# Optimization experiments

Measured on AMD Instinct MI355X. Metric: run time of the kernel, lower is better.

Reference implementation:

```python
import jax, jax.numpy as jnp
import numpy as np

B, I, H = 8192, 1024, 1024

def setup_inputs() -> dict:
    key = jax.random.key(0)
    ks = jax.random.split(key, 5)
    # xavier-uniform-ish scale for weights
    sW = float(np.sqrt(6.0 / (I + H)))
    sU = float(np.sqrt(6.0 / (H + H)))
    return {
        "x": jax.random.normal(ks[0], (B, I), jnp.float32),
        "h": jax.random.normal(ks[1], (B, H), jnp.float32),
        "c": jax.random.normal(ks[2], (B, H), jnp.float32),
        # gate order along leading axis: 0=i, 1=f, 2=o, 3=c_hat
        "W": jax.random.uniform(ks[3], (4, H, I), jnp.float32, -sW, sW),
        "bW": jnp.zeros((4, H), jnp.float32),
        "U": jax.random.uniform(ks[4], (4, H, H), jnp.float32, -sU, sU),
        "bU": jnp.zeros((4, H), jnp.float32),
    }

def reference(x, h, c, W, bW, U, bU):
    # two batched GEMMs covering all 8 original Linear layers
    gx = jnp.einsum('bi,ghi->gbh', x, W) + bW[:, None, :]   # [4,B,H]
    gh = jnp.einsum('bk,ghk->gbh', h, U) + bU[:, None, :]   # [4,B,H]
    g = gx + gh
    i = jax.nn.sigmoid(g[0])
    f = jax.nn.sigmoid(g[1])
    o = jax.nn.sigmoid(g[2])
    c_hat = jnp.tanh(g[3])
    c_new = f * c + i * c_hat
    h_new = o * jnp.tanh(c_new)
    return (h_new, (h_new, c_new))
```

## Files before the change

kernel.cpp:

```cpp
#include <hip/hip_runtime.h>
#include <hip/hip_bf16.h>

typedef __hip_bfloat16 bf16;
typedef __attribute__((ext_vector_type(8))) short short8;
typedef __attribute__((ext_vector_type(4))) float floatx4;

#define B_DIM 8192
#define H_DIM 1024
#define KSUM 2048
#define BM 128
#define BN 128
#define BK 64
#define KITER 32
#define CEX_STRIDE 68

union BS { bf16 b; short s; };
__device__ __forceinline__ short cvt1(float f) {
  BS u; u.b = __float2bfloat16(f); return u.s;
}
__device__ __forceinline__ short8 cvt8(float4 lo, float4 hi) {
  short8 r;
  r[0] = cvt1(lo.x); r[1] = cvt1(lo.y); r[2] = cvt1(lo.z); r[3] = cvt1(lo.w);
  r[4] = cvt1(hi.x); r[5] = cvt1(hi.y); r[6] = cvt1(hi.z); r[7] = cvt1(hi.w);
  return r;
}

__device__ __forceinline__ void async_ld16(const bf16* g, bf16* lds) {
  __builtin_amdgcn_global_load_lds(
      (const __attribute__((address_space(1))) unsigned int*)g,
      (__attribute__((address_space(3))) unsigned int*)lds,
      16, 0, 0);
}

__global__ __launch_bounds__(256) void cvt_pack_A(
    const float* __restrict__ x, const float* __restrict__ h,
    bf16* __restrict__ Ac) {
  const int idx = blockIdx.x * 256 + threadIdx.x;
  const long row = idx >> 8;
  const int k0 = (idx & 255) << 3;
  const float* src = (k0 < 1024) ? (x + row * 1024 + k0)
                                 : (h + row * 1024 + (k0 - 1024));
  const float4 lo = *(const float4*)src;
  const float4 hi = *(const float4*)(src + 4);
  *(short8*)(Ac + row * KSUM + k0) = cvt8(lo, hi);
}

__global__ __launch_bounds__(256) void cvt_pack_B(
    const float* __restrict__ W, const float* __restrict__ U,
    bf16* __restrict__ Bc) {
  const int idx = blockIdx.x * 256 + threadIdx.x;
  const long r = idx >> 8;
  const int k0 = (idx & 255) << 3;
  const int g = (int)(r & 3);
  const long hh = r >> 2;
  const long base = (long)g * (H_DIM * H_DIM) + hh * H_DIM;
  const float* src = (k0 < 1024) ? (W + base + k0) : (U + base + (k0 - 1024));
  const float4 lo = *(const float4*)src;
  const float4 hi = *(const float4*)(src + 4);
  *(short8*)(Bc + r * KSUM + k0) = cvt8(lo, hi);
}

__device__ __forceinline__ float sigmoidf_(float v) {
  return 1.0f / (1.0f + __expf(-v));
}
__device__ __forceinline__ float tanhf_(float v) {
  return 1.0f - 2.0f / (__expf(2.0f * v) + 1.0f);
}
__device__ __forceinline__ float getc(const float4& v, int t) {
  return t == 0 ? v.x : t == 1 ? v.y : t == 2 ? v.z : v.w;
}

__global__ __launch_bounds__(256) void gemm_lstm(
    const bf16* __restrict__ Ac, const bf16* __restrict__ Bc,
    const float* __restrict__ cprev_g, const float* __restrict__ bW,
    const float* __restrict__ bU, float* __restrict__ out) {
  __shared__ __align__(16) char smem[32768];
  bf16* sA = (bf16*)smem;
  bf16* sB = (bf16*)(smem + 16384);
  float* cex = (float*)smem;

  const int tid  = threadIdx.x;
  const int lane = tid & 63;
  const int wv   = tid >> 6;

  const int blk  = blockIdx.x;
  const int xcd  = blk & 7;
  const int slot = blk >> 3;
  const int mt   = slot & 63;
  const int nt   = (xcd << 2) | (slot >> 6);
  const long m0 = (long)mt * BM;
  const long n0 = (long)nt * BN;

  const int lrow   = lane >> 3;
  const int lchunk = lane & 7;
  const int schunk = lchunk ^ lrow;
  const bf16* aSrc = Ac + (m0 + wv * 8 + lrow) * (long)KSUM + schunk * 8;
  const bf16* bSrc = Bc + (n0 + wv * 8 + lrow) * (long)KSUM + schunk * 8;
  bf16* sAw = sA + (wv * 8) * 64;
  bf16* sBw = sB + (wv * 8) * 64;

  const int wm = ((wv >> 1) & 1) << 6;
  const int wn = (wv & 1) << 6;
  const int col16 = lane & 15;
  const int quad  = lane >> 4;
  const int x7    = col16 & 7;

  floatx4 acc[4][4];
#pragma unroll
  for (int i = 0; i < 4; ++i)
#pragma unroll
    for (int j = 0; j < 4; ++j) acc[i][j] = (floatx4){0.f, 0.f, 0.f, 0.f};

  for (int kt = 0; kt < KITER; ++kt) {
    const long koff = (long)kt * BK;
    __syncthreads();
#pragma unroll
    for (int q = 0; q < 4; ++q) {
      async_ld16(aSrc + koff + (long)q * (32 * (long)KSUM), sAw + q * (32 * 64));
      async_ld16(bSrc + koff + (long)q * (32 * (long)KSUM), sBw + q * (32 * 64));
    }
    __syncthreads();

#pragma unroll
    for (int s = 0; s < 2; ++s) {
      const int cp = ((((s << 2) + quad) ^ x7) << 3);
      short8 af[4], bfr[4];
#pragma unroll
      for (int i = 0; i < 4; ++i) {
        af[i]  = *(const short8*)&sA[(wm + i * 16 + col16) * 64 + cp];
        bfr[i] = *(const short8*)&sB[(wn + i * 16 + col16) * 64 + cp];
      }
#pragma unroll
      for (int i = 0; i < 4; ++i)
#pragma unroll
        for (int j = 0; j < 4; ++j)
          acc[i][j] = __builtin_amdgcn_mfma_f32_16x16x32_bf16(af[i], bfr[j],
                                                              acc[i][j], 0, 0, 0);
    }
  }

  __syncthreads();

  const int rquad = (lane >> 4) << 2;
  const int row16 = lane & 15;
  const int tq    = lane >> 4;
  const long hglob = (n0 >> 2) + (wn >> 2) + tq * 4;

  float4 bsum[4];
#pragma unroll
  for (int g = 0; g < 4; ++g) {
    const float4 a = *(const float4*)(bW + g * H_DIM + hglob);
    const float4 b = *(const float4*)(bU + g * H_DIM + hglob);
    bsum[g] = (float4){a.x + b.x, a.y + b.y, a.z + b.z, a.w + b.w};
  }

  float* wx = cex + wv * (16 * CEX_STRIDE);
  const long BH = (long)B_DIM * H_DIM;

  for (int ig = 0; ig < 4; ++ig) {
#pragma unroll
    for (int j = 0; j < 4; ++j)
#pragma unroll
      for (int r = 0; r < 4; ++r)
        wx[(rquad + r) * CEX_STRIDE + j * 16 + col16] = acc[ig][j][r];

    float4 g4[4];
#pragma unroll
    for (int t = 0; t < 4; ++t)
      g4[t] = *(const float4*)&wx[row16 * CEX_STRIDE + (tq * 4 + t) * 4];

    const long mrow = m0 + wm + ig * 16 + row16;
    const float4 cp4 = *(const float4*)(cprev_g + mrow * H_DIM + hglob);

    float hn[4], cn[4];
#pragma unroll
    for (int t = 0; t < 4; ++t) {
      const float gi = g4[t].x + getc(bsum[0], t);
      const float gf = g4[t].y + getc(bsum[1], t);
      const float go = g4[t].z + getc(bsum[2], t);
      const float gg = g4[t].w + getc(bsum[3], t);
      const float I = sigmoidf_(gi);
      const float F = sigmoidf_(gf);
      const float O = sigmoidf_(go);
      const float G = tanhf_(gg);
      const float cv = F * getc(cp4, t) + I * G;
      hn[t] = O * tanhf_(cv);
      cn[t] = cv;
    }
    const float4 hn4 = {hn[0], hn[1], hn[2], hn[3]};
    const float4 cn4 = {cn[0], cn[1], cn[2], cn[3]};
    const long ob = mrow * H_DIM + hglob;
    *(float4*)(out + ob)          = hn4;
    *(float4*)(out + BH + ob)     = hn4;
    *(float4*)(out + 2 * BH + ob) = cn4;
  }
}

extern "C" void kernel_launch(void* const* d_in, const int* in_sizes, int n_in,
                              void* d_out, int out_size, void* d_ws, size_t ws_size,
                              hipStream_t stream) {
  const float* x  = (const float*)d_in[0];
  const float* h  = (const float*)d_in[1];
  const float* c  = (const float*)d_in[2];
  const float* W  = (const float*)d_in[3];
  const float* bW = (const float*)d_in[4];
  const float* U  = (const float*)d_in[5];
  const float* bU = (const float*)d_in[6];
  float* out = (float*)d_out;

  bf16* Ac = (bf16*)d_ws;
  bf16* Bc = (bf16*)((char*)d_ws + (size_t)33554432);

  cvt_pack_A<<<8192, 256, 0, stream>>>(x, h, Ac);
  cvt_pack_B<<<4096, 256, 0, stream>>>(W, U, Bc);
  gemm_lstm<<<2048, 256, 0, stream>>>(Ac, Bc, c, bW, bU, out);
}
```

Before: 394.2 us.

## Double-buffer LDS tiles in GEMM and merge the two conversion kernels

The GEMM main loop now uses two LDS buffers for the A and B tiles. Async global-to-LDS loads for the next K tile are issued before the MFMA work on the current tile, so memory latency can overlap with compute and one barrier pair per iteration goes away. LDS per block doubles to 64KB, which may cut the number of resident blocks per CU. The A and B fp32-to-bf16 pack kernels are also merged into one launch that branches on block index, saving a kernel launch.

```diff
diff --git a/kernel.cpp b/kernel.cpp
--- a/kernel.cpp
+++ b/kernel.cpp
@@ -32,32 +32,32 @@
       16, 0, 0);
 }
 
-__global__ __launch_bounds__(256) void cvt_pack_A(
+__global__ __launch_bounds__(256) void cvt_pack(
     const float* __restrict__ x, const float* __restrict__ h,
-    bf16* __restrict__ Ac) {
-  const int idx = blockIdx.x * 256 + threadIdx.x;
-  const long row = idx >> 8;
-  const int k0 = (idx & 255) << 3;
-  const float* src = (k0 < 1024) ? (x + row * 1024 + k0)
-                                 : (h + row * 1024 + (k0 - 1024));
-  const float4 lo = *(const float4*)src;
-  const float4 hi = *(const float4*)(src + 4);
-  *(short8*)(Ac + row * KSUM + k0) = cvt8(lo, hi);
-}
-
-__global__ __launch_bounds__(256) void cvt_pack_B(
     const float* __restrict__ W, const float* __restrict__ U,
-    bf16* __restrict__ Bc) {
-  const int idx = blockIdx.x * 256 + threadIdx.x;
-  const long r = idx >> 8;
-  const int k0 = (idx & 255) << 3;
-  const int g = (int)(r & 3);
-  const long hh = r >> 2;
-  const long base = (long)g * (H_DIM * H_DIM) + hh * H_DIM;
-  const float* src = (k0 < 1024) ? (W + base + k0) : (U + base + (k0 - 1024));
-  const float4 lo = *(const float4*)src;
-  const float4 hi = *(const float4*)(src + 4);
-  *(short8*)(Bc + r * KSUM + k0) = cvt8(lo, hi);
+    bf16* __restrict__ Ac, bf16* __restrict__ Bc) {
+  const int blk = blockIdx.x;
+  if (blk < 8192) {
+    const int idx = blk * 256 + threadIdx.x;
+    const long row = idx >> 8;
+    const int k0 = (idx & 255) << 3;
+    const float* src = (k0 < 1024) ? (x + row * 1024 + k0)
+                                   : (h + row * 1024 + (k0 - 1024));
+    const float4 lo = *(const float4*)src;
+    const float4 hi = *(const float4*)(src + 4);
+    *(short8*)(Ac + row * KSUM + k0) = cvt8(lo, hi);
+  } else {
+    const int idx = (blk - 8192) * 256 + threadIdx.x;
+    const long r = idx >> 8;
+    const int k0 = (idx & 255) << 3;
+    const int g = (int)(r & 3);
+    const long hh = r >> 2;
+    const long base = (long)g * (H_DIM * H_DIM) + hh * H_DIM;
+    const float* src = (k0 < 1024) ? (W + base + k0) : (U + base + (k0 - 1024));
+    const float4 lo = *(const float4*)src;
+    const float4 hi = *(const float4*)(src + 4);
+    *(short8*)(Bc + r * KSUM + k0) = cvt8(lo, hi);
+  }
 }
 
 __device__ __forceinline__ float sigmoidf_(float v) {
@@ -74,10 +74,12 @@
     const bf16* __restrict__ Ac, const bf16* __restrict__ Bc,
     const float* __restrict__ cprev_g, const float* __restrict__ bW,
     const float* __restrict__ bU, float* __restrict__ out) {
-  __shared__ __align__(16) char smem[32768];
-  bf16* sA = (bf16*)smem;
-  bf16* sB = (bf16*)(smem + 16384);
-  float* cex = (float*)smem;
+  __shared__ __align__(16) char smem[65536];
+  bf16* const sA0 = (bf16*)smem;
+  bf16* const sB0 = (bf16*)(smem + 16384);
+  bf16* const sA1 = (bf16*)(smem + 32768);
+  bf16* const sB1 = (bf16*)(smem + 49152);
+  float* const cex = (float*)smem;
 
   const int tid  = threadIdx.x;
   const int lane = tid & 63;
@@ -96,8 +98,10 @@
   const int schunk = lchunk ^ lrow;
   const bf16* aSrc = Ac + (m0 + wv * 8 + lrow) * (long)KSUM + schunk * 8;
   const bf16* bSrc = Bc + (n0 + wv * 8 + lrow) * (long)KSUM + schunk * 8;
-  bf16* sAw = sA + (wv * 8) * 64;
-  bf16* sBw = sB + (wv * 8) * 64;
+  bf16* const dA0 = sA0 + wv * 512;
+  bf16* const dB0 = sB0 + wv * 512;
+  bf16* const dA1 = sA1 + wv * 512;
+  bf16* const dB1 = sB1 + wv * 512;
 
   const int wm = ((wv >> 1) & 1) << 6;
   const int wn = (wv & 1) << 6;
@@ -111,32 +115,45 @@
 #pragma unroll
     for (int j = 0; j < 4; ++j) acc[i][j] = (floatx4){0.f, 0.f, 0.f, 0.f};
 
-  for (int kt = 0; kt < KITER; ++kt) {
-    const long koff = (long)kt * BK;
+#define STAGE(kt, dA, dB)                                                 \
+  {                                                                       \
+    const long koff_ = (long)(kt) * BK;                                   \
+    _Pragma("unroll")                                                     \
+    for (int q = 0; q < 4; ++q) {                                         \
+      async_ld16(aSrc + koff_ + (long)q * (32 * (long)KSUM), (dA) + q * 2048); \
+      async_ld16(bSrc + koff_ + (long)q * (32 * (long)KSUM), (dB) + q * 2048); \
+    }                                                                     \
+  }
+
+#define COMPUTE(sAp, sBp)                                                 \
+  {                                                                       \
+    _Pragma("unroll")                                                     \
+    for (int s = 0; s < 2; ++s) {                                         \
+      const int cp = ((((s << 2) + quad) ^ x7) << 3);                     \
+      short8 af[4], bfr[4];                                               \
+      _Pragma("unroll")                                                   \
+      for (int i = 0; i < 4; ++i) {                                       \
+        af[i]  = *(const short8*)&(sAp)[(wm + i * 16 + col16) * 64 + cp]; \
+        bfr[i] = *(const short8*)&(sBp)[(wn + i * 16 + col16) * 64 + cp]; \
+      }                                                                   \
+      _Pragma("unroll")                                                   \
+      for (int i = 0; i < 4; ++i)                                         \
+        _Pragma("unroll")                                                 \
+        for (int j = 0; j < 4; ++j)                                       \
+          acc[i][j] = __builtin_amdgcn_mfma_f32_16x16x32_bf16(            \
+              af[i], bfr[j], acc[i][j], 0, 0, 0);                         \
+    }                                                                     \
+  }
+
+  STAGE(0, dA0, dB0);
+#pragma unroll 1
+  for (int kt = 0; kt < KITER; kt += 2) {
     __syncthreads();
-#pragma unroll
-    for (int q = 0; q < 4; ++q) {
-      async_ld16(aSrc + koff + (long)q * (32 * (long)KSUM), sAw + q * (32 * 64));
-      async_ld16(bSrc + koff + (long)q * (32 * (long)KSUM), sBw + q * (32 * 64));
-    }
+    STAGE(kt + 1, dA1, dB1);
+    COMPUTE(sA0, sB0);
     __syncthreads();
-
-#pragma unroll
-    for (int s = 0; s < 2; ++s) {
-      const int cp = ((((s << 2) + quad) ^ x7) << 3);
-      short8 af[4], bfr[4];
-#pragma unroll
-      for (int i = 0; i < 4; ++i) {
-        af[i]  = *(const short8*)&sA[(wm + i * 16 + col16) * 64 + cp];
-        bfr[i] = *(const short8*)&sB[(wn + i * 16 + col16) * 64 + cp];
-      }
-#pragma unroll
-      for (int i = 0; i < 4; ++i)
-#pragma unroll
-        for (int j = 0; j < 4; ++j)
-          acc[i][j] = __builtin_amdgcn_mfma_f32_16x16x32_bf16(af[i], bfr[j],
-                                                              acc[i][j], 0, 0, 0);
-    }
+    if (kt + 2 < KITER) STAGE(kt + 2, dA0, dB0);
+    COMPUTE(sA1, sB1);
   }
 
   __syncthreads();
@@ -211,7 +228,6 @@
   bf16* Ac = (bf16*)d_ws;
   bf16* Bc = (bf16*)((char*)d_ws + (size_t)33554432);
 
-  cvt_pack_A<<<8192, 256, 0, stream>>>(x, h, Ac);
-  cvt_pack_B<<<4096, 256, 0, stream>>>(W, U, Bc);
+  cvt_pack<<<12288, 256, 0, stream>>>(x, h, W, U, Ac, Bc);
   gemm_lstm<<<2048, 256, 0, stream>>>(Ac, Bc, c, bW, bU, out);
 }
```

Result: faster. 376.7 us (-4.4%).
